# Performance work log

Measured on AMD Instinct MI355X. Metric: run time of the kernel, lower is better.

Reference implementation:

```python
import jax, jax.numpy as jnp
import numpy as np

DIM = 128
HEADS = 8
K_RATIO = 0.5
LAYER_SCALE = 0.1
EPS = 1e-6


def setup_inputs() -> dict:
    key = jax.random.key(0)
    ks = jax.random.split(key, 18)
    d = DIM
    hd3 = d * 3  # high-frequency channels (lh,hl,hh)
    f = lambda k, shape, s=0.05: jax.random.normal(k, shape, dtype=jnp.float32) * s
    return {
        "x": jax.random.normal(ks[0], (8, d, 64, 64), dtype=jnp.float32),
        "qkv_w": f(ks[1], (3 * d, d)),
        "proj_w": f(ks[2], (d, d)),
        "attn_gn_g": 1.0 + f(ks[3], (d,)),
        "attn_gn_b": f(ks[4], (d,)),
        "he_dw_w": f(ks[5], (hd3, 1, 3, 3)),
        "he_gn1_g": 1.0 + f(ks[6], (hd3,)),
        "he_gn1_b": f(ks[7], (hd3,)),
        "he_pw_w": f(ks[8], (hd3, hd3)),
        "he_gn2_g": 1.0 + f(ks[9], (hd3,)),
        "he_gn2_b": f(ks[10], (hd3,)),
        "alpha": jnp.array([0.1], dtype=jnp.float32),
        "ffn_w1": f(ks[11], (2 * d, d)),
        "ffn_gn1_g": 1.0 + f(ks[12], (2 * d,)),
        "ffn_gn1_b": f(ks[13], (2 * d,)),
        "ffn_w2": f(ks[14], (d, 2 * d)),
        "ffn_gn2_g": 1.0 + f(ks[15], (d,)),
        "ffn_gn2_b": f(ks[16], (d,)),
    }


def _group_norm(x, g, b, groups):
    B, C, H, W = x.shape
    xg = x.reshape(B, groups, -1)
    mu = xg.mean(-1, keepdims=True)
    var = xg.var(-1, keepdims=True)
    xn = ((xg - mu) * jax.lax.rsqrt(var + EPS)).reshape(B, C, H, W)
    return xn * g[:, None, None] + b[:, None, None]


def _conv1x1(x, w):
    return jnp.einsum('oc,bchw->bohw', w, x)


def _l2norm(t):
    # matches F.normalize(dim=-1, eps=1e-12): x / norm.clamp_min(eps)
    return t / jnp.maximum(jnp.linalg.norm(t, axis=-1, keepdims=True), 1e-12)


def _sparse_attn(ll, qkv_w, proj_w, g, b):
    B, C, H, W = ll.shape
    N = H * W
    nh = HEADS
    hd = C // nh
    scale = hd ** -0.5
    qkv = _conv1x1(ll, qkv_w).reshape(B, 3, nh, hd, N)
    q = jnp.swapaxes(qkv[:, 0], -1, -2)  # [B,nh,N,hd]
    k = jnp.swapaxes(qkv[:, 1], -1, -2)
    v = jnp.swapaxes(qkv[:, 2], -1, -2)
    q = _l2norm(q)
    k = _l2norm(k)
    attn = jnp.einsum('bhnd,bhmd->bhnm', q, k) * scale  # [B,nh,N,N]
    attn = jnp.clip(attn, -32.0, 32.0)  # fp32 clamp value
    k_num = max(int(N * K_RATIO), 1)
    if k_num < N:
        _, idx = jax.lax.top_k(attn, k_num)  # [B,nh,N,k_num]
        flat_attn = attn.reshape(-1, N)
        rows = jnp.arange(flat_attn.shape[0])[:, None]
        mask = jnp.zeros(flat_attn.shape, dtype=bool).at[rows, idx.reshape(-1, k_num)].set(True)
        attn = jnp.where(mask.reshape(attn.shape), attn, jnp.float32(-1e9))
    attn = jax.nn.softmax(attn, axis=-1)
    out = jnp.einsum('bhnm,bhmd->bhnd', attn, v)
    out = jnp.swapaxes(out, 2, 3).reshape(B, C, H, W)
    out = _conv1x1(out, proj_w)
    return _group_norm(out, g, b, min(32, C // 4))


def _high_enhance(h, dw_w, g1, b1, pw_w, g2, b2, alpha):
    C = h.shape[1]
    groups = min(32, C // 8)
    y = jax.lax.conv_general_dilated(
        h, dw_w, window_strides=(1, 1), padding='SAME',
        feature_group_count=C, dimension_numbers=('NCHW', 'OIHW', 'NCHW'))
    y = jax.nn.silu(_group_norm(y, g1, b1, groups))
    y = _group_norm(_conv1x1(y, pw_w), g2, b2, groups)
    return h + alpha[0] * y


def _iwt(ll, lh, hl, hh):
    a = ll - lh - hl + hh  # goes to (even row, even col)
    bq = ll - lh + hl - hh  # (odd row, even col)
    c = ll + lh - hl - hh  # (even row, odd col)
    d = ll + lh + hl + hh  # (odd row, odd col)
    B, C, H, W = ll.shape
    row_even = jnp.stack([a, c], axis=-1)  # [B,C,H,W,2] col parity
    row_odd = jnp.stack([bq, d], axis=-1)
    h = jnp.stack([row_even, row_odd], axis=3)  # [B,C,H,2,W,2]
    return h.reshape(B, C, 2 * H, 2 * W)


def _ffn(x, w1, g1, b1, w2, g2, b2):
    d = x.shape[1]
    groups = min(32, d // 4)
    y = _group_norm(_conv1x1(x, w1), g1, b1, groups)
    y = jax.nn.gelu(y, approximate=False)
    return _group_norm(_conv1x1(y, w2), g2, b2, groups)


def reference(x, qkv_w, proj_w, attn_gn_g, attn_gn_b,
              he_dw_w, he_gn1_g, he_gn1_b, he_pw_w, he_gn2_g, he_gn2_b, alpha,
              ffn_w1, ffn_gn1_g, ffn_gn1_b, ffn_w2, ffn_gn2_g, ffn_gn2_b):
    # DWT (Haar, stride-2 slicing)
    x1 = x[:, :, 0::2, 0::2]
    x2 = x[:, :, 1::2, 0::2]
    x3 = x[:, :, 0::2, 1::2]
    x4 = x[:, :, 1::2, 1::2]
    ll = (x1 + x2 + x3 + x4) * 0.5
    lh = (-x1 - x2 + x3 + x4) * 0.5
    hl = (-x1 + x2 - x3 + x4) * 0.5
    hh = (x1 - x2 - x3 + x4) * 0.5
    high = jnp.concatenate([lh, hl, hh], axis=1)

    ll_out = _sparse_attn(ll, qkv_w, proj_w, attn_gn_g, attn_gn_b)
    high_out = _high_enhance(high, he_dw_w, he_gn1_g, he_gn1_b, he_pw_w, he_gn2_g, he_gn2_b, alpha)

    C = ll.shape[1]
    x_rec = _iwt(ll + ll_out, high_out[:, :C], high_out[:, C:2 * C], high_out[:, 2 * C:])

    out = x + LAYER_SCALE * x_rec
    out = out + LAYER_SCALE * _ffn(out, ffn_w1, ffn_gn1_g, ffn_gn1_b, ffn_w2, ffn_gn2_g, ffn_gn2_b)
    return out
```

## Files before the change

kernel.cpp:

```cpp
#include <hip/hip_runtime.h>
#include <cstdint>
#include <cstddef>

#define BB 8
#define CC 128
#define C3 384
#define HH 64
#define H2 32
#define NPIX 1024
#define N4 4096
#define NHD 8
#define HD 16

typedef _Float16 h2f __attribute__((ext_vector_type(2)));
typedef _Float16 h4f __attribute__((ext_vector_type(4)));
typedef float f4 __attribute__((ext_vector_type(4)));

union U4H { uint4 u; h2f h[4]; };
union H4U { h4f v; h2f h[2]; };

__device__ inline h2f pkrtz(float a, float b) {
  return __builtin_bit_cast(h2f, __builtin_amdgcn_cvt_pkrtz(a, b));
}

__global__ __launch_bounds__(256) void k_dwt(const float* __restrict__ x,
                                             float* __restrict__ ll,
                                             float* __restrict__ high) {
  int idx = blockIdx.x * 256 + threadIdx.x;
  int w = idx & 31, h = (idx >> 5) & 31, c = (idx >> 10) & 127, b = idx >> 17;
  const float* xp = x + ((size_t)(b * CC + c) * HH + 2 * h) * HH + 2 * w;
  float x1 = xp[0];
  float x2 = xp[HH];
  float x3 = xp[1];
  float x4 = xp[HH + 1];
  int n = h * H2 + w;
  ll[(size_t)(b * CC + c) * NPIX + n]              = 0.5f * ( x1 + x2 + x3 + x4);
  high[((size_t)b * C3 + c) * NPIX + n]            = 0.5f * (-x1 - x2 + x3 + x4);
  high[((size_t)b * C3 + CC + c) * NPIX + n]       = 0.5f * (-x1 + x2 - x3 + x4);
  high[((size_t)b * C3 + 2 * CC + c) * NPIX + n]   = 0.5f * ( x1 - x2 - x3 + x4);
}

template <int CIN, int P, int OPT, bool SWZ = false>
__global__ __launch_bounds__(256) void k_conv1x1(const float* __restrict__ in,
                                                 const float* __restrict__ w,
                                                 float* __restrict__ out,
                                                 int Cout, int Npix) {
  int tid = threadIdx.x;
  int n0, o0, b;
  if constexpr (SWZ) {
    int L = blockIdx.x;
    int low = L & 31;
    b = low >> 2;
    n0 = ((low & 3) * 256 + tid) * P;
    o0 = (L >> 5) * OPT;
  } else {
    n0 = (blockIdx.x * 256 + tid) * P;
    o0 = blockIdx.y * OPT;
    b = blockIdx.z;
  }
  const float* inb = in + (size_t)b * CIN * Npix + n0;
  const float* wb = w + (size_t)o0 * CIN;
  float acc[OPT][P];
#pragma unroll
  for (int o = 0; o < OPT; ++o)
#pragma unroll
    for (int p = 0; p < P; ++p) acc[o][p] = 0.f;

  for (int c0 = 0; c0 < CIN; c0 += 8) {
#pragma unroll
    for (int c = 0; c < 8; ++c) {
      float vv[P];
      const float* ip = inb + (size_t)(c0 + c) * Npix;
      if constexpr (P == 4) {
        float4 t = *(const float4*)ip;
        vv[0] = t.x; vv[1] = t.y; vv[2] = t.z; vv[3] = t.w;
      } else if constexpr (P == 2) {
        float2 t = *(const float2*)ip;
        vv[0] = t.x; vv[1] = t.y;
      } else {
        vv[0] = ip[0];
      }
#pragma unroll
      for (int o = 0; o < OPT; ++o) {
        float wc = wb[(size_t)o * CIN + c0 + c];
#pragma unroll
        for (int p = 0; p < P; ++p) acc[o][p] = fmaf(wc, vv[p], acc[o][p]);
      }
    }
  }
  size_t ob = ((size_t)b * Cout + o0) * Npix + n0;
#pragma unroll
  for (int o = 0; o < OPT; ++o) {
    float* op = out + ob + (size_t)o * Npix;
    if constexpr (P == 4) {
      *(float4*)op = make_float4(acc[o][0], acc[o][1], acc[o][2], acc[o][3]);
    } else if constexpr (P == 2) {
      *(float2*)op = make_float2(acc[o][0], acc[o][1]);
    } else {
      op[0] = acc[o][0];
    }
  }
}

__global__ __launch_bounds__(256) void k_qkvnorm(const float* __restrict__ qkv,
                                                 uint4* __restrict__ qh,
                                                 uint4* __restrict__ kh,
                                                 uint16_t* __restrict__ vt) {
  __shared__ uint16_t lds_v[16 * 256];
  int tid = threadIdx.x;
  int idx = blockIdx.x * 256 + tid;
  int n = idx & 1023, h = (idx >> 10) & 7, b = idx >> 13;
  const float* base = qkv + ((size_t)b * C3 + h * HD) * NPIX + n;
  float q[HD], k[HD], vv[HD];
  float sq = 0.f, sk = 0.f;
#pragma unroll
  for (int d = 0; d < HD; ++d) {
    q[d] = base[(size_t)d * NPIX];
    k[d] = base[(size_t)(CC + d) * NPIX];
    vv[d] = base[(size_t)(2 * CC + d) * NPIX];
    sq += q[d] * q[d];
    sk += k[d] * k[d];
  }
  float rq = 1.f / fmaxf(sqrtf(sq), 1e-12f);
  float rk = 1.f / fmaxf(sqrtf(sk), 1e-12f);
#pragma unroll
  for (int g = 0; g < 2; ++g) {
    U4H pq, pk;
#pragma unroll
    for (int d = 0; d < 4; ++d) {
      int e = g * 8 + 2 * d;
      pq.h[d] = pkrtz(q[e] * rq, q[e + 1] * rq);
      pk.h[d] = pkrtz(k[e] * rk, k[e + 1] * rk);
    }
    qh[(size_t)idx * 2 + g] = pq.u;
    kh[(size_t)idx * 2 + g] = pk.u;
  }
#pragma unroll
  for (int d = 0; d < HD; ++d) {
    union { _Float16 f; uint16_t u; } cv;
    cv.f = (_Float16)vv[d];
    lds_v[d * 256 + tid] = cv.u;
  }
  __syncthreads();
  int bh = idx >> 10;
  int n0 = (blockIdx.x * 256) & 1023;
  const uint32_t* ldw = (const uint32_t*)lds_v;
  uint32_t* vtw = (uint32_t*)(vt + (size_t)bh * 16384 + n0);
#pragma unroll
  for (int r = 0; r < 8; ++r) {
    int d = 2 * r + (tid >> 7);
    int c = tid & 127;
    vtw[(size_t)d * 512 + c] = ldw[d * 128 + c];
  }
}

__global__ __launch_bounds__(256) void k_attn(const uint16_t* __restrict__ qh,
                                              const uint16_t* __restrict__ kh,
                                              const uint16_t* __restrict__ vt,
                                              float* __restrict__ attn_out) {
  __shared__ int cnt_lds[12 * 64];
  __shared__ float sum_lds[64];
  __shared__ f4 obuf[4 * 64];
  int tid = threadIdx.x;
  int lane = tid & 63;
  int w = tid >> 6;
  int blk = blockIdx.x;
  int bh = blk >> 6;
  int q0 = (blk & 63) << 4;
  int lm = lane & 15;
  int lg = lane >> 4;
  int b = bh >> 3, h = bh & 7;

  H4U bq;
  bq.v = *(const h4f*)(qh + ((size_t)bh * 1024 + q0 + lm) * 16 + 4 * lg);
  const h2f qsc = {(_Float16)0.25f, (_Float16)0.25f};
  bq.h[0] *= qsc;
  bq.h[1] *= qsc;

  const f4 z = {0.f, 0.f, 0.f, 0.f};
  const uint16_t* kbase = kh + (size_t)bh * 16384 + 4 * lg;
  h2f sc[16][2];
#pragma unroll
  for (int j = 0; j < 16; ++j) {
    int J = (w << 4) | j;
    h4f ak = *(const h4f*)(kbase + (size_t)(16 * J + lm) * 16);
    f4 d = __builtin_amdgcn_mfma_f32_16x16x16f16(ak, bq.v, z, 0, 0, 0);
    sc[j][0] = pkrtz(d[0], d[1]);
    sc[j][1] = pkrtz(d[2], d[3]);
  }

  float lo = -0.26f, hi = 0.26f;
  _Float16 hlo = (_Float16)(-0.26f);
#pragma unroll 1
  for (int it = 0; it < 12; ++it) {
    float mid = 0.5f * (lo + hi);
    _Float16 hm = (_Float16)mid;
    int c = 0;
#pragma unroll
    for (int j = 0; j < 16; ++j) {
      c += (sc[j][0][0] >= hm);
      c += (sc[j][0][1] >= hm);
      c += (sc[j][1][0] >= hm);
      c += (sc[j][1][1] >= hm);
    }
    c += __shfl_xor(c, 16);
    c += __shfl_xor(c, 32);
    if (lg == 0) cnt_lds[it * 64 + lm * 4 + w] = c;
    __syncthreads();
    int4 c4 = *(const int4*)&cnt_lds[it * 64 + lm * 4];
    int ct = (c4.x + c4.y) + (c4.z + c4.w);
    bool ge = (ct >= 512);
    lo = ge ? mid : lo;
    hlo = ge ? hm : hlo;
    hi = ge ? hi : mid;
  }

  float ss = 0.f;
#pragma unroll
  for (int j = 0; j < 16; ++j) {
#pragma unroll
    for (int r = 0; r < 2; ++r) {
      h2f t = sc[j][r];
      float p0 = (t[0] >= hlo) ? __expf((float)t[0]) : 0.f;
      float p1 = (t[1] >= hlo) ? __expf((float)t[1]) : 0.f;
      ss += p0 + p1;
      sc[j][r] = pkrtz(p0, p1);
    }
  }
  ss += __shfl_xor(ss, 16);
  ss += __shfl_xor(ss, 32);
  if (lg == 0) sum_lds[lm * 4 + w] = ss;
  __syncthreads();
  float4 s4 = *(const float4*)&sum_lds[lm * 4];
  float inv = 1.f / ((s4.x + s4.y) + (s4.z + s4.w));

  const uint16_t* vbase = vt + (size_t)bh * 16384 + (size_t)lm * 1024 + 4 * lg;
  f4 acc[2] = {z, z};
#pragma unroll
  for (int j = 0; j < 16; ++j) {
    int J = (w << 4) | j;
    h4f va = *(const h4f*)(vbase + 16 * J);
    H4U pf;
    pf.h[0] = sc[j][0];
    pf.h[1] = sc[j][1];
    acc[j & 1] = __builtin_amdgcn_mfma_f32_16x16x16f16(va, pf.v, acc[j & 1], 0, 0, 0);
  }
  f4 o = acc[0] + acc[1];
  obuf[(w << 6) | lane] = o;
  __syncthreads();
  if (w == 0) {
    f4 t = obuf[lane] + obuf[64 + lane] + obuf[128 + lane] + obuf[192 + lane];
#pragma unroll
    for (int e = 0; e < 4; ++e) {
      int dim = 4 * lg + e;
      attn_out[((size_t)(b * CC + h * HD + dim) * NPIX) + q0 + lm] = t[e] * inv;
    }
  }
}

__global__ __launch_bounds__(512) void k_dwgn(const float* __restrict__ in,
                                              const float* __restrict__ w,
                                              float* __restrict__ out,
                                              const float* __restrict__ gamma,
                                              const float* __restrict__ beta) {
  __shared__ float xs[12 * 1152];
  __shared__ float sred[8], s2red[8];
  int blk = blockIdx.x;
  int b = blk & 7, g = blk >> 3;
  int tid = threadIdx.x;
  int c0 = g * 12;
  const float* inb = in + ((size_t)b * C3 + c0) * NPIX;
#pragma unroll
  for (int k = 0; k < 6; ++k) {
    int e = (k * 512 + tid) * 4;
    int cc = e >> 10, rem = e & 1023;
    int row = rem >> 5, col = rem & 31;
    float4 v = *(const float4*)(inb + e);
    *(float4*)&xs[cc * 1152 + row * 36 + col] = v;
  }
  __syncthreads();
  int n0 = tid * 2;
  int i = n0 >> 5, j0 = n0 & 31;
  float acc[12][2];
  float s = 0.f, s2 = 0.f;
#pragma unroll
  for (int cc = 0; cc < 12; ++cc) {
    const float* wc = w + (size_t)(c0 + cc) * 9;
    float w0 = wc[0], w1 = wc[1], w2 = wc[2], w3 = wc[3], w4 = wc[4],
          w5 = wc[5], w6 = wc[6], w7 = wc[7], w8 = wc[8];
    float r[3][4];
#pragma unroll
    for (int di = 0; di < 3; ++di) {
      int ii = i + di - 1;
      bool rv = (ii >= 0 && ii < 32);
#pragma unroll
      for (int dj = 0; dj < 4; ++dj) {
        int jj = j0 + dj - 1;
        r[di][dj] = (rv && jj >= 0 && jj < 32) ? xs[cc * 1152 + ii * 36 + jj] : 0.f;
      }
    }
#pragma unroll
    for (int p = 0; p < 2; ++p) {
      float a = r[0][p] * w0 + r[0][p + 1] * w1 + r[0][p + 2] * w2
              + r[1][p] * w3 + r[1][p + 1] * w4 + r[1][p + 2] * w5
              + r[2][p] * w6 + r[2][p + 1] * w7 + r[2][p + 2] * w8;
      acc[cc][p] = a;
      s += a;
      s2 += a * a;
    }
  }
#pragma unroll
  for (int off = 32; off > 0; off >>= 1) {
    s += __shfl_xor(s, off);
    s2 += __shfl_xor(s2, off);
  }
  int wv = tid >> 6;
  if ((tid & 63) == 0) { sred[wv] = s; s2red[wv] = s2; }
  __syncthreads();
  float st = 0.f, s2t = 0.f;
#pragma unroll
  for (int k = 0; k < 8; ++k) { st += sred[k]; s2t += s2red[k]; }
  float inv_n = 1.f / 12288.f;
  float mean = st * inv_n;
  float var = s2t * inv_n - mean * mean;
  float rstd = rsqrtf(var + 1e-6f);
#pragma unroll
  for (int cc = 0; cc < 12; ++cc) {
    float2 o;
#pragma unroll
    for (int p = 0; p < 2; ++p) {
      float gnv = (acc[cc][p] - mean) * rstd * gamma[c0 + cc] + beta[c0 + cc];
      ((float*)&o)[p] = gnv / (1.f + __expf(-gnv));
    }
    *(float2*)(out + ((size_t)b * C3 + c0 + cc) * NPIX + n0) = o;
  }
}

__global__ __launch_bounds__(1024) void k_pwgn(const float* __restrict__ in,
                                               const float* __restrict__ w,
                                               const float* __restrict__ res,
                                               float* __restrict__ out,
                                               const float* __restrict__ gamma,
                                               const float* __restrict__ beta,
                                               const float* __restrict__ alpha_ptr) {
  __shared__ float wl[12 * 384];
  __shared__ float sred[16], s2red[16];
  int blk = blockIdx.x;
  int b = blk & 7, g = blk >> 3;
  int tid = threadIdx.x;
  int c0 = g * 12;
  const float* wsrc = w + (size_t)c0 * C3;
  for (int k = tid; k < 12 * 384; k += 1024) wl[k] = wsrc[k];
  __syncthreads();
  const float* inb = in + (size_t)b * C3 * NPIX + tid;
  float acc[12];
#pragma unroll
  for (int o = 0; o < 12; ++o) acc[o] = 0.f;
#pragma unroll 4
  for (int c = 0; c < 384; ++c) {
    float v = inb[(size_t)c * NPIX];
#pragma unroll
    for (int o = 0; o < 12; ++o) acc[o] = fmaf(wl[o * 384 + c], v, acc[o]);
  }
  float s = 0.f, s2 = 0.f;
#pragma unroll
  for (int o = 0; o < 12; ++o) { s += acc[o]; s2 += acc[o] * acc[o]; }
#pragma unroll
  for (int off = 32; off > 0; off >>= 1) {
    s += __shfl_xor(s, off);
    s2 += __shfl_xor(s2, off);
  }
  int wv = tid >> 6;
  if ((tid & 63) == 0) { sred[wv] = s; s2red[wv] = s2; }
  __syncthreads();
  float st = 0.f, s2t = 0.f;
#pragma unroll
  for (int k = 0; k < 16; ++k) { st += sred[k]; s2t += s2red[k]; }
  float inv_n = 1.f / 12288.f;
  float mean = st * inv_n;
  float var = s2t * inv_n - mean * mean;
  float rstd = rsqrtf(var + 1e-6f);
  float a = alpha_ptr[0];
#pragma unroll
  for (int o = 0; o < 12; ++o) {
    size_t base = ((size_t)b * C3 + c0 + o) * NPIX + tid;
    out[base] = res[base] + a * ((acc[o] - mean) * rstd * gamma[c0 + o] + beta[c0 + o]);
  }
}

__global__ __launch_bounds__(1024) void k_ffn1(const float* __restrict__ in,
                                               const float* __restrict__ w,
                                               float* __restrict__ out,
                                               const float* __restrict__ gamma,
                                               const float* __restrict__ beta) {
  __shared__ float wl[8 * 128];
  __shared__ float sred[16], s2red[16];
  int blk = blockIdx.x;
  int b = blk & 7, g = blk >> 3;
  int tid = threadIdx.x;
  int c0 = g * 8;
  const float* wsrc = w + (size_t)c0 * CC;
  if (tid < 1024) wl[tid] = wsrc[tid];
  __syncthreads();
  const float* inb = in + (size_t)b * CC * N4 + tid * 4;
  float acc[8][4];
#pragma unroll
  for (int o = 0; o < 8; ++o)
#pragma unroll
    for (int p = 0; p < 4; ++p) acc[o][p] = 0.f;
#pragma unroll 4
  for (int c = 0; c < 128; ++c) {
    float4 v = *(const float4*)(inb + (size_t)c * N4);
#pragma unroll
    for (int o = 0; o < 8; ++o) {
      float wv = wl[o * 128 + c];
      acc[o][0] = fmaf(wv, v.x, acc[o][0]);
      acc[o][1] = fmaf(wv, v.y, acc[o][1]);
      acc[o][2] = fmaf(wv, v.z, acc[o][2]);
      acc[o][3] = fmaf(wv, v.w, acc[o][3]);
    }
  }
  float s = 0.f, s2 = 0.f;
#pragma unroll
  for (int o = 0; o < 8; ++o)
#pragma unroll
    for (int p = 0; p < 4; ++p) { s += acc[o][p]; s2 += acc[o][p] * acc[o][p]; }
#pragma unroll
  for (int off = 32; off > 0; off >>= 1) {
    s += __shfl_xor(s, off);
    s2 += __shfl_xor(s2, off);
  }
  int wv = tid >> 6;
  if ((tid & 63) == 0) { sred[wv] = s; s2red[wv] = s2; }
  __syncthreads();
  float st = 0.f, s2t = 0.f;
#pragma unroll
  for (int k = 0; k < 16; ++k) { st += sred[k]; s2t += s2red[k]; }
  float inv_n = 1.f / 32768.f;
  float mean = st * inv_n;
  float var = s2t * inv_n - mean * mean;
  float rstd = rsqrtf(var + 1e-6f);
#pragma unroll
  for (int o = 0; o < 8; ++o) {
    float gm = gamma[c0 + o], bt = beta[c0 + o];
    float r[4];
#pragma unroll
    for (int p = 0; p < 4; ++p) {
      float gnv = (acc[o][p] - mean) * rstd * gm + bt;
      r[p] = 0.5f * gnv * (1.f + erff(gnv * 0.70710678118654752f));
    }
    *(float4*)(out + ((size_t)(b * 256 + c0 + o)) * N4 + tid * 4) =
        make_float4(r[0], r[1], r[2], r[3]);
  }
}

template <int ITER, int ACT, bool HAS_RES>
__global__ __launch_bounds__(512) void k_gnr(const float* __restrict__ x,
                                             const float* __restrict__ res,
                                             float* __restrict__ out,
                                             const float* __restrict__ gamma,
                                             const float* __restrict__ beta,
                                             float alpha_const,
                                             int chPerGroup, int Npix, int nshift) {
  int g = blockIdx.x & 31, b = blockIdx.x >> 5;
  int Cout = 32 * chPerGroup;
  int elems = chPerGroup * Npix;
  size_t base = ((size_t)b * Cout + g * chPerGroup) * Npix;
  const float4* xv = (const float4*)(x + base);
  int tid = threadIdx.x;
  float4 xc[ITER];
  float s = 0.f, s2 = 0.f;
#pragma unroll
  for (int k = 0; k < ITER; ++k) {
    float4 v = xv[tid + k * 512];
    xc[k] = v;
    s += v.x + v.y + v.z + v.w;
    s2 += v.x * v.x + v.y * v.y + v.z * v.z + v.w * v.w;
  }
#pragma unroll
  for (int off = 32; off > 0; off >>= 1) {
    s += __shfl_xor(s, off);
    s2 += __shfl_xor(s2, off);
  }
  __shared__ float ls[8], ls2[8];
  int wv = tid >> 6, ln = tid & 63;
  if (ln == 0) { ls[wv] = s; ls2[wv] = s2; }
  __syncthreads();
  float st = 0.f, s2t = 0.f;
#pragma unroll
  for (int k = 0; k < 8; ++k) { st += ls[k]; s2t += ls2[k]; }
  float inv_n = 1.f / (float)elems;
  float mean = st * inv_n;
  float var = s2t * inv_n - mean * mean;
  float rstd = rsqrtf(var + 1e-6f);
  const float4* rv = (const float4*)(res + base);
  float4* ov = (float4*)(out + base);
  int cshift = nshift - 2;
#pragma unroll
  for (int k = 0; k < ITER; ++k) {
    int i = tid + k * 512;
    int cc = g * chPerGroup + (i >> cshift);
    float gm = gamma[cc], bt = beta[cc];
    float4 v = xc[k];
    float r[4] = {v.x, v.y, v.z, v.w};
#pragma unroll
    for (int p = 0; p < 4; ++p) {
      float gnv = (r[p] - mean) * rstd * gm + bt;
      if (ACT == 1)      r[p] = gnv / (1.f + __expf(-gnv));
      else if (ACT == 2) r[p] = 0.5f * gnv * (1.f + erff(gnv * 0.70710678118654752f));
      else               r[p] = gnv;
    }
    float4 o;
    if (HAS_RES) {
      float4 rr = rv[i];
      o = make_float4(rr.x + alpha_const * r[0], rr.y + alpha_const * r[1],
                      rr.z + alpha_const * r[2], rr.w + alpha_const * r[3]);
    } else {
      o = make_float4(r[0], r[1], r[2], r[3]);
    }
    ov[i] = o;
  }
}

__global__ __launch_bounds__(256) void k_iwt(const float* __restrict__ x,
                                             const float* __restrict__ s1,
                                             const float* __restrict__ hout,
                                             float* __restrict__ out) {
  int idx = blockIdx.x * 256 + threadIdx.x;
  int w = idx & 31, h = (idx >> 5) & 31, c = (idx >> 10) & 127, b = idx >> 17;
  int n = h * 32 + w;
  float ll = s1[(size_t)(b * CC + c) * NPIX + n];
  float lh = hout[((size_t)b * C3 + c) * NPIX + n];
  float hl = hout[((size_t)b * C3 + CC + c) * NPIX + n];
  float hh = hout[((size_t)b * C3 + 2 * CC + c) * NPIX + n];
  float va = ll - lh - hl + hh;
  float vb = ll - lh + hl - hh;
  float vc = ll + lh - hl - hh;
  float vd = ll + lh + hl + hh;
  size_t xb = ((size_t)(b * CC + c) * HH + 2 * h) * HH + 2 * w;
  out[xb]          = x[xb]          + 0.1f * va;
  out[xb + 1]      = x[xb + 1]      + 0.1f * vc;
  out[xb + HH]     = x[xb + HH]     + 0.1f * vb;
  out[xb + HH + 1] = x[xb + HH + 1] + 0.1f * vd;
}

extern "C" void kernel_launch(void* const* d_in, const int* in_sizes, int n_in,
                              void* d_out, int out_size, void* d_ws, size_t ws_size,
                              hipStream_t stream) {
  const float* x         = (const float*)d_in[0];
  const float* qkv_w     = (const float*)d_in[1];
  const float* proj_w    = (const float*)d_in[2];
  const float* attn_gn_g = (const float*)d_in[3];
  const float* attn_gn_b = (const float*)d_in[4];
  const float* he_dw_w   = (const float*)d_in[5];
  const float* he_gn1_g  = (const float*)d_in[6];
  const float* he_gn1_b  = (const float*)d_in[7];
  const float* he_pw_w   = (const float*)d_in[8];
  const float* he_gn2_g  = (const float*)d_in[9];
  const float* he_gn2_b  = (const float*)d_in[10];
  const float* alpha     = (const float*)d_in[11];
  const float* ffn_w1    = (const float*)d_in[12];
  const float* ffn_gn1_g = (const float*)d_in[13];
  const float* ffn_gn1_b = (const float*)d_in[14];
  const float* ffn_w2    = (const float*)d_in[15];
  const float* ffn_gn2_g = (const float*)d_in[16];
  const float* ffn_gn2_b = (const float*)d_in[17];
  float* out = (float*)d_out;

  float* ws = (float*)d_ws;
  float* ll   = ws;
  float* high = ws + 1048576;
  float* qkv  = ws + 4194304;
  float* qnkv = ws + 7340032;
  float* atto = ws + 10485760;
  float* proj = ws + 11534336;
  float* f1   = ws + 12582912;
  float* f3   = ws + 20971520;
  uint4* qh = (uint4*)qnkv;
  uint4* kh = (uint4*)(qnkv + 524288);
  uint16_t* vt = (uint16_t*)(qnkv + 1048576);
  float* y1 = qkv;
  float* pw = qnkv;

  k_dwt<<<4096, 256, 0, stream>>>(x, ll, high);
  k_conv1x1<128, 1, 8><<<dim3(4, 48, 8), 256, 0, stream>>>(ll, qkv_w, qkv, 384, 1024);
  k_qkvnorm<<<256, 256, 0, stream>>>(qkv, qh, kh, vt);
  k_attn<<<4096, 256, 0, stream>>>((const uint16_t*)qh, (const uint16_t*)kh, vt, atto);
  k_conv1x1<128, 1, 4><<<dim3(4, 32, 8), 256, 0, stream>>>(atto, proj_w, proj, 128, 1024);
  k_gnr<2, 0, true><<<256, 512, 0, stream>>>(proj, ll, proj, attn_gn_g, attn_gn_b,
                                             1.0f, 4, 1024, 10);
  k_dwgn<<<256, 512, 0, stream>>>(high, he_dw_w, y1, he_gn1_g, he_gn1_b);
  k_pwgn<<<256, 1024, 0, stream>>>(y1, he_pw_w, high, pw, he_gn2_g, he_gn2_b, alpha);
  k_iwt<<<4096, 256, 0, stream>>>(x, proj, pw, out);
  k_ffn1<<<256, 1024, 0, stream>>>(out, ffn_w1, f1, ffn_gn1_g, ffn_gn1_b);
  k_conv1x1<256, 4, 8, true><<<512, 256, 0, stream>>>(f1, ffn_w2, f3, 128, 4096);
  k_gnr<8, 0, true><<<256, 512, 0, stream>>>(f3, out, out, ffn_gn2_g, ffn_gn2_b,
                                             0.1f, 4, 4096, 12);
  (void)in_sizes; (void)n_in; (void)out_size; (void)ws_size;
}
```

Measured before the change: 384.9 us.

## Fuse proj and FFN2 1x1 convs with their GroupNorm-residual epilogues

Replaces the separate proj conv + k_gnr and FFN second conv + k_gnr pairs with single kernels, k_projgn and k_ffn2gn. In each, one block computes a full GroupNorm group (4 output channels × all pixels), reduces the statistics in-block and writes the normalized residual output directly. This removes the intermediate proj/f3 round trips through global memory and two launches. In exchange each block reads the whole input channel stack for only 4 output channels, so input reuse across output channels drops. The grid also shrinks to 256 blocks of 1024 threads, which may limit latency hiding on the conv.

Result: no change. 385.1 us (+0.0%).

```diff
diff --git a/kernel.cpp b/kernel.cpp
--- a/kernel.cpp
+++ b/kernel.cpp
@@ -40,24 +40,15 @@
   high[((size_t)b * C3 + 2 * CC + c) * NPIX + n]   = 0.5f * ( x1 - x2 - x3 + x4);
 }
 
-template <int CIN, int P, int OPT, bool SWZ = false>
+template <int CIN, int P, int OPT>
 __global__ __launch_bounds__(256) void k_conv1x1(const float* __restrict__ in,
                                                  const float* __restrict__ w,
                                                  float* __restrict__ out,
                                                  int Cout, int Npix) {
   int tid = threadIdx.x;
-  int n0, o0, b;
-  if constexpr (SWZ) {
-    int L = blockIdx.x;
-    int low = L & 31;
-    b = low >> 2;
-    n0 = ((low & 3) * 256 + tid) * P;
-    o0 = (L >> 5) * OPT;
-  } else {
-    n0 = (blockIdx.x * 256 + tid) * P;
-    o0 = blockIdx.y * OPT;
-    b = blockIdx.z;
-  }
+  int n0 = (blockIdx.x * 256 + tid) * P;
+  int o0 = blockIdx.y * OPT;
+  int b = blockIdx.z;
   const float* inb = in + (size_t)b * CIN * Npix + n0;
   const float* wb = w + (size_t)o0 * CIN;
   float acc[OPT][P];
@@ -258,6 +249,54 @@
   }
 }
 
+__global__ __launch_bounds__(1024) void k_projgn(const float* __restrict__ in,
+                                                 const float* __restrict__ w,
+                                                 const float* __restrict__ res,
+                                                 float* __restrict__ out,
+                                                 const float* __restrict__ gamma,
+                                                 const float* __restrict__ beta) {
+  __shared__ float wl[4 * 128];
+  __shared__ float sred[16], s2red[16];
+  int blk = blockIdx.x;
+  int b = blk & 7, g = blk >> 3;
+  int tid = threadIdx.x;
+  int c0 = g * 4;
+  const float* wsrc = w + (size_t)c0 * CC;
+  if (tid < 512) wl[tid] = wsrc[tid];
+  __syncthreads();
+  const float* inb = in + (size_t)b * CC * NPIX + tid;
+  float acc[4] = {0.f, 0.f, 0.f, 0.f};
+#pragma unroll 8
+  for (int c = 0; c < 128; ++c) {
+    float v = inb[(size_t)c * NPIX];
+#pragma unroll
+    for (int o = 0; o < 4; ++o) acc[o] = fmaf(wl[o * 128 + c], v, acc[o]);
+  }
+  float s = 0.f, s2 = 0.f;
+#pragma unroll
+  for (int o = 0; o < 4; ++o) { s += acc[o]; s2 += acc[o] * acc[o]; }
+#pragma unroll
+  for (int off = 32; off > 0; off >>= 1) {
+    s += __shfl_xor(s, off);
+    s2 += __shfl_xor(s2, off);
+  }
+  int wv = tid >> 6;
+  if ((tid & 63) == 0) { sred[wv] = s; s2red[wv] = s2; }
+  __syncthreads();
+  float st = 0.f, s2t = 0.f;
+#pragma unroll
+  for (int k = 0; k < 16; ++k) { st += sred[k]; s2t += s2red[k]; }
+  float inv_n = 1.f / 4096.f;
+  float mean = st * inv_n;
+  float var = s2t * inv_n - mean * mean;
+  float rstd = rsqrtf(var + 1e-6f);
+#pragma unroll
+  for (int o = 0; o < 4; ++o) {
+    size_t base = ((size_t)b * CC + c0 + o) * NPIX + tid;
+    out[base] = res[base] + ((acc[o] - mean) * rstd * gamma[c0 + o] + beta[c0 + o]);
+  }
+}
+
 __global__ __launch_bounds__(512) void k_dwgn(const float* __restrict__ in,
                                               const float* __restrict__ w,
                                               float* __restrict__ out,
@@ -454,71 +493,69 @@
   }
 }
 
-template <int ITER, int ACT, bool HAS_RES>
-__global__ __launch_bounds__(512) void k_gnr(const float* __restrict__ x,
-                                             const float* __restrict__ res,
-                                             float* __restrict__ out,
-                                             const float* __restrict__ gamma,
-                                             const float* __restrict__ beta,
-                                             float alpha_const,
-                                             int chPerGroup, int Npix, int nshift) {
-  int g = blockIdx.x & 31, b = blockIdx.x >> 5;
-  int Cout = 32 * chPerGroup;
-  int elems = chPerGroup * Npix;
-  size_t base = ((size_t)b * Cout + g * chPerGroup) * Npix;
-  const float4* xv = (const float4*)(x + base);
-  int tid = threadIdx.x;
-  float4 xc[ITER];
+__global__ __launch_bounds__(1024) void k_ffn2gn(const float* __restrict__ in,
+                                                 const float* __restrict__ w,
+                                                 float* __restrict__ out,
+                                                 const float* __restrict__ gamma,
+                                                 const float* __restrict__ beta) {
+  __shared__ float wl[4 * 256];
+  __shared__ float sred[16], s2red[16];
+  int blk = blockIdx.x;
+  int b = blk & 7, g = blk >> 3;
+  int tid = threadIdx.x;
+  int c0 = g * 4;
+  const float* wsrc = w + (size_t)c0 * 256;
+  if (tid < 1024) wl[tid] = wsrc[tid];
+  __syncthreads();
+  const float* inb = in + (size_t)b * 256 * N4 + tid * 4;
+  float acc[4][4];
+#pragma unroll
+  for (int o = 0; o < 4; ++o)
+#pragma unroll
+    for (int p = 0; p < 4; ++p) acc[o][p] = 0.f;
+#pragma unroll 4
+  for (int c = 0; c < 256; ++c) {
+    float4 v = *(const float4*)(inb + (size_t)c * N4);
+#pragma unroll
+    for (int o = 0; o < 4; ++o) {
+      float wv = wl[o * 256 + c];
+      acc[o][0] = fmaf(wv, v.x, acc[o][0]);
+      acc[o][1] = fmaf(wv, v.y, acc[o][1]);
+      acc[o][2] = fmaf(wv, v.z, acc[o][2]);
+      acc[o][3] = fmaf(wv, v.w, acc[o][3]);
+    }
+  }
   float s = 0.f, s2 = 0.f;
 #pragma unroll
-  for (int k = 0; k < ITER; ++k) {
-    float4 v = xv[tid + k * 512];
-    xc[k] = v;
-    s += v.x + v.y + v.z + v.w;
-    s2 += v.x * v.x + v.y * v.y + v.z * v.z + v.w * v.w;
-  }
+  for (int o = 0; o < 4; ++o)
+#pragma unroll
+    for (int p = 0; p < 4; ++p) { s += acc[o][p]; s2 += acc[o][p] * acc[o][p]; }
 #pragma unroll
   for (int off = 32; off > 0; off >>= 1) {
     s += __shfl_xor(s, off);
     s2 += __shfl_xor(s2, off);
   }
-  __shared__ float ls[8], ls2[8];
-  int wv = tid >> 6, ln = tid & 63;
-  if (ln == 0) { ls[wv] = s; ls2[wv] = s2; }
+  int wv = tid >> 6;
+  if ((tid & 63) == 0) { sred[wv] = s; s2red[wv] = s2; }
   __syncthreads();
   float st = 0.f, s2t = 0.f;
 #pragma unroll
-  for (int k = 0; k < 8; ++k) { st += ls[k]; s2t += ls2[k]; }
-  float inv_n = 1.f / (float)elems;
+  for (int k = 0; k < 16; ++k) { st += sred[k]; s2t += s2red[k]; }
+  float inv_n = 1.f / 16384.f;
   float mean = st * inv_n;
   float var = s2t * inv_n - mean * mean;
   float rstd = rsqrtf(var + 1e-6f);
-  const float4* rv = (const float4*)(res + base);
-  float4* ov = (float4*)(out + base);
-  int cshift = nshift - 2;
-#pragma unroll
-  for (int k = 0; k < ITER; ++k) {
-    int i = tid + k * 512;
-    int cc = g * chPerGroup + (i >> cshift);
-    float gm = gamma[cc], bt = beta[cc];
-    float4 v = xc[k];
-    float r[4] = {v.x, v.y, v.z, v.w};
-#pragma unroll
-    for (int p = 0; p < 4; ++p) {
-      float gnv = (r[p] - mean) * rstd * gm + bt;
-      if (ACT == 1)      r[p] = gnv / (1.f + __expf(-gnv));
-      else if (ACT == 2) r[p] = 0.5f * gnv * (1.f + erff(gnv * 0.70710678118654752f));
-      else               r[p] = gnv;
-    }
-    float4 o;
-    if (HAS_RES) {
-      float4 rr = rv[i];
-      o = make_float4(rr.x + alpha_const * r[0], rr.y + alpha_const * r[1],
-                      rr.z + alpha_const * r[2], rr.w + alpha_const * r[3]);
-    } else {
-      o = make_float4(r[0], r[1], r[2], r[3]);
-    }
-    ov[i] = o;
+#pragma unroll
+  for (int o = 0; o < 4; ++o) {
+    float gm = gamma[c0 + o], bt = beta[c0 + o];
+    float* op = out + ((size_t)(b * CC + c0 + o)) * N4 + tid * 4;
+    float4 rr = *(const float4*)op;
+    float4 ov;
+    ov.x = rr.x + 0.1f * ((acc[o][0] - mean) * rstd * gm + bt);
+    ov.y = rr.y + 0.1f * ((acc[o][1] - mean) * rstd * gm + bt);
+    ov.z = rr.z + 0.1f * ((acc[o][2] - mean) * rstd * gm + bt);
+    ov.w = rr.w + 0.1f * ((acc[o][3] - mean) * rstd * gm + bt);
+    *(float4*)op = ov;
   }
 }
 
@@ -575,7 +612,6 @@
   float* atto = ws + 10485760;
   float* proj = ws + 11534336;
   float* f1   = ws + 12582912;
-  float* f3   = ws + 20971520;
   uint4* qh = (uint4*)qnkv;
   uint4* kh = (uint4*)(qnkv + 524288);
   uint16_t* vt = (uint16_t*)(qnkv + 1048576);
@@ -586,15 +622,11 @@
   k_conv1x1<128, 1, 8><<<dim3(4, 48, 8), 256, 0, stream>>>(ll, qkv_w, qkv, 384, 1024);
   k_qkvnorm<<<256, 256, 0, stream>>>(qkv, qh, kh, vt);
   k_attn<<<4096, 256, 0, stream>>>((const uint16_t*)qh, (const uint16_t*)kh, vt, atto);
-  k_conv1x1<128, 1, 4><<<dim3(4, 32, 8), 256, 0, stream>>>(atto, proj_w, proj, 128, 1024);
-  k_gnr<2, 0, true><<<256, 512, 0, stream>>>(proj, ll, proj, attn_gn_g, attn_gn_b,
-                                             1.0f, 4, 1024, 10);
+  k_projgn<<<256, 1024, 0, stream>>>(atto, proj_w, ll, proj, attn_gn_g, attn_gn_b);
   k_dwgn<<<256, 512, 0, stream>>>(high, he_dw_w, y1, he_gn1_g, he_gn1_b);
   k_pwgn<<<256, 1024, 0, stream>>>(y1, he_pw_w, high, pw, he_gn2_g, he_gn2_b, alpha);
   k_iwt<<<4096, 256, 0, stream>>>(x, proj, pw, out);
   k_ffn1<<<256, 1024, 0, stream>>>(out, ffn_w1, f1, ffn_gn1_g, ffn_gn1_b);
-  k_conv1x1<256, 4, 8, true><<<512, 256, 0, stream>>>(f1, ffn_w2, f3, 128, 4096);
-  k_gnr<8, 0, true><<<256, 512, 0, stream>>>(f3, out, out, ffn_gn2_g, ffn_gn2_b,
-                                             0.1f, 4, 4096, 12);
+  k_ffn2gn<<<256, 1024, 0, stream>>>(f1, ffn_w2, out, ffn_gn2_g, ffn_gn2_b);
   (void)in_sizes; (void)n_in; (void)out_size; (void)ws_size;
 }
```
